# Kernel optimization log

Hardware: AMD Instinct MI355X
Metric: run time of the kernel (lower is better)

## Reference

```python
import jax, jax.numpy as jnp
import numpy as np

B, S, D, H = 4, 2048, 1024, 16
HD = D // H


def setup_inputs() -> dict:
    key = jax.random.key(0)
    ks = jax.random.split(key, 11)
    s = 1.0 / np.sqrt(D)
    inp = {
        "query": jax.random.normal(ks[0], (B, S, D), jnp.float32),
        "key": jax.random.normal(ks[1], (B, S, D), jnp.float32),
        "value": jax.random.normal(ks[2], (B, S, D), jnp.float32),
        "Wq": jax.random.normal(ks[3], (D, D), jnp.float32) * s,
        "bq": jnp.zeros((D,), jnp.float32),
        "Wk": jax.random.normal(ks[4], (D, D), jnp.float32) * s,
        "bk": jnp.zeros((D,), jnp.float32),
        "Wv": jax.random.normal(ks[5], (D, D), jnp.float32) * s,
        "bv": jnp.zeros((D,), jnp.float32),
        "Wo": jax.random.normal(ks[6], (D, D), jnp.float32) * s,
        "bo": jnp.zeros((D,), jnp.float32),
    }
    return inp


def reference(query, key, value, Wq, bq, Wk, bk, Wv, bv, Wo, bo):
    scale = 1.0 / np.sqrt(HD).astype(np.float32)
    # Linear projections (torch Linear: x @ W.T + b), split into heads -> [B,H,S,HD]
    def proj(x, W, b):
        y = x @ W.T + b
        return y.reshape(B, S, H, HD).transpose(0, 2, 1, 3)

    q = proj(query, Wq, bq)
    k = proj(key, Wk, bk)
    v = proj(value, Wv, bv)
    scores = jnp.einsum("bhqd,bhkd->bhqk", q, k) * scale  # [B,H,S,S]
    weights = jax.nn.softmax(scores, axis=-1)
    attn = jnp.einsum("bhqk,bhkd->bhqd", weights, v)
    attn = attn.transpose(0, 2, 1, 3).reshape(B, S, D)
    return attn @ Wo.T + bo
```

## Files before the change

kernel.cpp:

```cpp
#include <hip/hip_runtime.h>
#include <hip/hip_bf16.h>
#include <stdint.h>

#define Bn 4
#define Sn 2048
#define Dn 1024
#define Hn 16
#define HDn 64
#define Mn (Bn * Sn)
#define PS 44

typedef __attribute__((ext_vector_type(8))) __bf16 bf16x8;
typedef __attribute__((ext_vector_type(4))) __bf16 bf16x4;
typedef __attribute__((ext_vector_type(4))) float f32x4;

#if __has_builtin(__builtin_amdgcn_exp2f)
#define EXP2F(x) __builtin_amdgcn_exp2f(x)
#else
#define EXP2F(x) exp2f(x)
#endif

typedef __attribute__((address_space(1))) unsigned int as1_uint;
typedef __attribute__((address_space(3))) unsigned int as3_uint;

__device__ __forceinline__ void gld_lds16(const void* g, void* l) {
  __builtin_amdgcn_global_load_lds((const as1_uint*)g, (as3_uint*)l, 16, 0, 0);
}

struct CvtArgs {
  const float* src[7];
};
__constant__ const size_t kGb[8] = {0,       1048576, 2097152, 3145728,
                                    3276800, 3407872, 3538944, 3670016};

__global__ __launch_bounds__(256) void cvt_all(CvtArgs a, __bf16* __restrict__ dst) {
  size_t i = (size_t)blockIdx.x * 256 + threadIdx.x;
  if (i >= 3670016) return;
  int s = 0;
#pragma unroll
  for (int k = 1; k < 7; k++) s += (i >= kGb[k]) ? 1 : 0;
  const float4* sp = (const float4*)a.src[s] + 2 * (i - kGb[s]);
  float4 x = sp[0], y = sp[1];
  bf16x8 o;
  o[0] = (__bf16)x.x; o[1] = (__bf16)x.y; o[2] = (__bf16)x.z; o[3] = (__bf16)x.w;
  o[4] = (__bf16)y.x; o[5] = (__bf16)y.y; o[6] = (__bf16)y.z; o[7] = (__bf16)y.w;
  *(bf16x8*)(dst + 8 * i) = o;
}

template <int MODE>
__device__ __forceinline__ void gemm128_body(const __bf16* __restrict__ A,
                                             const __bf16* __restrict__ Bw,
                                             const float* __restrict__ bias,
                                             void* __restrict__ Cout, int m0, int n0,
                                             float scale) {
  __shared__ __align__(16) __bf16 lA[128 * 32];
  __shared__ __align__(16) __bf16 lB[128 * 32];
  const int tid = threadIdx.x;
  const int wave = tid >> 6, lane = tid & 63, quad = lane >> 4, l15 = lane & 15;
  const int wm = wave >> 1, wn = wave & 1;
  f32x4 acc[4][4] = {};
  const char* Ab = (const char*)(A + (size_t)m0 * Dn);
  const char* Bb = (const char*)(Bw + (size_t)n0 * Dn);
  char* lAc = (char*)lA;
  char* lBc = (char*)lB;
  const int o0 = tid * 16, o1 = o0 + 4096;
  const int r0 = o0 >> 6, c0 = o0 & 63;
  const int r1 = o1 >> 6, c1 = o1 & 63;

  for (int k0 = 0; k0 < Dn; k0 += 32) {
    __syncthreads();
    gld_lds16(Ab + (size_t)r0 * 2048 + k0 * 2 + c0, lAc + o0);
    gld_lds16(Ab + (size_t)r1 * 2048 + k0 * 2 + c1, lAc + o1);
    gld_lds16(Bb + (size_t)r0 * 2048 + k0 * 2 + c0, lBc + o0);
    gld_lds16(Bb + (size_t)r1 * 2048 + k0 * 2 + c1, lBc + o1);
    __syncthreads();
    bf16x8 af[4], bfv[4];
#pragma unroll
    for (int i = 0; i < 4; i++)
      af[i] = *(const bf16x8*)(lA + (wm * 64 + i * 16 + l15) * 32 + quad * 8);
#pragma unroll
    for (int t = 0; t < 4; t++)
      bfv[t] = *(const bf16x8*)(lB + (wn * 64 + t * 16 + l15) * 32 + quad * 8);
#pragma unroll
    for (int i = 0; i < 4; i++)
#pragma unroll
      for (int t = 0; t < 4; t++)
        acc[i][t] = __builtin_amdgcn_mfma_f32_16x16x32_bf16(af[i], bfv[t], acc[i][t], 0, 0, 0);
  }
#pragma unroll
  for (int i = 0; i < 4; i++) {
    const int rowb = m0 + wm * 64 + i * 16 + quad * 4;
#pragma unroll
    for (int t = 0; t < 4; t++) {
      const int col = n0 + wn * 64 + t * 16 + l15;
      const float bb = bias[col];
      if (MODE == 2) {
        const int b = rowb >> 11, s = rowb & 2047;
        const int h = col >> 6, c = col & 63;
        bf16x4 pk;
#pragma unroll
        for (int r = 0; r < 4; r++) pk[r] = (__bf16)(acc[i][t][r] + bb);
        *(bf16x4*)((__bf16*)Cout + (((size_t)(b * Hn + h) * HDn + c) * Sn + s)) = pk;
      } else {
#pragma unroll
        for (int r = 0; r < 4; r++) {
          float v = (acc[i][t][r] + bb) * scale;
          if (MODE == 1)
            ((float*)Cout)[(size_t)(rowb + r) * Dn + col] = v;
          else
            ((__bf16*)Cout)[(size_t)(rowb + r) * Dn + col] = (__bf16)v;
        }
      }
    }
  }
}

__global__ __launch_bounds__(256, 3) void qkv_gemm(
    const __bf16* __restrict__ X, const __bf16* __restrict__ W,
    const float* __restrict__ bq, const float* __restrict__ bk,
    const float* __restrict__ bv, __bf16* __restrict__ out) {
  const int z = blockIdx.z;
  const int m0 = blockIdx.y * 128, n0 = blockIdx.x * 128;
  if (z == 0) {
    gemm128_body<0>(X, W, bq, out, m0, n0, 0.18033688011112042f);
  } else if (z == 1) {
    gemm128_body<0>(X + (size_t)Mn * Dn, W + (size_t)Dn * Dn, bk,
                    out + (size_t)Mn * Dn, m0, n0, 1.0f);
  } else {
    gemm128_body<2>(X + 2 * (size_t)Mn * Dn, W + 2 * (size_t)Dn * Dn, bv,
                    out + 2 * (size_t)Mn * Dn, m0, n0, 1.0f);
  }
}

__global__ __launch_bounds__(256, 3) void out_gemm(const __bf16* __restrict__ A,
                                                   const __bf16* __restrict__ W,
                                                   const float* __restrict__ bo,
                                                   float* __restrict__ out) {
  gemm128_body<1>(A, W, bo, out, blockIdx.y * 128, blockIdx.x * 128, 1.0f);
}

__global__ __launch_bounds__(256, 2) void flash_attn(const __bf16* __restrict__ Q,
                                                     const __bf16* __restrict__ K,
                                                     const __bf16* __restrict__ Vt,
                                                     __bf16* __restrict__ Aout) {
  __shared__ __align__(16) __bf16 plds[4][64 * PS];
  const int tid = threadIdx.x;
  const int wave = tid >> 6, lane = tid & 63, quad = lane >> 4, l15 = lane & 15;
  const int b = blockIdx.y >> 4, h = blockIdx.y & 15;
  const int q0 = blockIdx.x * 256 + wave * 64;
  const __bf16* Qb = Q + ((size_t)b * Sn) * Dn + h * HDn;
  const __bf16* Kb = K + ((size_t)b * Sn) * Dn + h * HDn;
  const __bf16* Vtb = Vt + (size_t)(b * Hn + h) * HDn * Sn;
  __bf16* myP = &plds[wave][0];

  bf16x8 qf[4][2];
#pragma unroll
  for (int iq = 0; iq < 4; iq++)
#pragma unroll
    for (int s = 0; s < 2; s++)
      qf[iq][s] = *(const bf16x8*)(Qb + (size_t)(q0 + iq * 16 + l15) * Dn + s * 32 + quad * 8);

  f32x4 O[4][4] = {};
  float li[4] = {};

  bf16x8 kf[2][2][2];
  bf16x8 vf[2][4];
#pragma unroll
  for (int tk = 0; tk < 2; tk++)
#pragma unroll
    for (int s = 0; s < 2; s++)
      kf[0][tk][s] = *(const bf16x8*)(Kb + (size_t)(tk * 16 + l15) * Dn + s * 32 + quad * 8);
#pragma unroll
  for (int mc = 0; mc < 4; mc++)
    vf[0][mc] = *(const bf16x8*)(Vtb + (size_t)(mc * 16 + l15) * Sn + quad * 8);

#pragma unroll 2
  for (int kt = 0; kt < Sn / 32; kt++) {
    const int cur = kt & 1, nxt = cur ^ 1;
    f32x4 sa[2][4];
#pragma unroll
    for (int tk = 0; tk < 2; tk++)
#pragma unroll
      for (int iq = 0; iq < 4; iq++) {
        f32x4 z = {0.f, 0.f, 0.f, 0.f};
        z = __builtin_amdgcn_mfma_f32_16x16x32_bf16(kf[cur][tk][0], qf[iq][0], z, 0, 0, 0);
        z = __builtin_amdgcn_mfma_f32_16x16x32_bf16(kf[cur][tk][1], qf[iq][1], z, 0, 0, 0);
        sa[tk][iq] = z;
      }
    if (kt < Sn / 32 - 1) {
      const int key0 = (kt + 1) * 32;
#pragma unroll
      for (int tk = 0; tk < 2; tk++)
#pragma unroll
        for (int s = 0; s < 2; s++)
          kf[nxt][tk][s] =
              *(const bf16x8*)(Kb + (size_t)(key0 + tk * 16 + l15) * Dn + s * 32 + quad * 8);
#pragma unroll
      for (int mc = 0; mc < 4; mc++)
        vf[nxt][mc] = *(const bf16x8*)(Vtb + (size_t)(mc * 16 + l15) * Sn + key0 + quad * 8);
    }
#pragma unroll
    for (int tk = 0; tk < 2; tk++)
#pragma unroll
      for (int iq = 0; iq < 4; iq++) {
        bf16x4 pk;
#pragma unroll
        for (int r = 0; r < 4; r++) {
          float p = EXP2F(sa[tk][iq][r]);
          li[iq] += p;
          pk[r] = (__bf16)p;
        }
        *(bf16x4*)(myP + (iq * 16 + l15) * PS + tk * 16 + quad * 4) = pk;
      }
#pragma unroll
    for (int iq = 0; iq < 4; iq++) {
      bf16x4 plo = *(const bf16x4*)(myP + (iq * 16 + l15) * PS + quad * 8);
      bf16x4 phi = *(const bf16x4*)(myP + (iq * 16 + l15) * PS + quad * 8 + 4);
      bf16x8 pf = __builtin_shufflevector(plo, phi, 0, 1, 2, 3, 4, 5, 6, 7);
#pragma unroll
      for (int mc = 0; mc < 4; mc++)
        O[mc][iq] = __builtin_amdgcn_mfma_f32_16x16x32_bf16(vf[cur][mc], pf, O[mc][iq], 0, 0, 0);
    }
  }
  float inv[4];
#pragma unroll
  for (int iq = 0; iq < 4; iq++) {
    float s = li[iq];
    s += __shfl_xor(s, 16);
    s += __shfl_xor(s, 32);
    inv[iq] = 1.0f / s;
  }
#pragma unroll
  for (int mc = 0; mc < 4; mc++)
#pragma unroll
    for (int iq = 0; iq < 4; iq++) {
      bf16x4 o;
#pragma unroll
      for (int r = 0; r < 4; r++) o[r] = (__bf16)(O[mc][iq][r] * inv[iq]);
      *(bf16x4*)(Aout + ((size_t)b * Sn + q0 + iq * 16 + l15) * Dn + h * HDn + mc * 16 +
                 quad * 4) = o;
    }
}

extern "C" void kernel_launch(void* const* d_in, const int* in_sizes, int n_in,
                              void* d_out, int out_size, void* d_ws, size_t ws_size,
                              hipStream_t stream) {
  const float* bq = (const float*)d_in[4];
  const float* bk = (const float*)d_in[6];
  const float* bv = (const float*)d_in[8];
  const float* bo = (const float*)d_in[10];

  const size_t MD = (size_t)Mn * Dn;
  const size_t DD = (size_t)Dn * Dn;
  __bf16* Xbf  = (__bf16*)d_ws;
  __bf16* Wbf  = Xbf + 3 * MD;
  __bf16* QKV  = Wbf + 4 * DD;
  __bf16* Attn = QKV + 3 * MD;

  CvtArgs ca;
  ca.src[0] = (const float*)d_in[0];
  ca.src[1] = (const float*)d_in[1];
  ca.src[2] = (const float*)d_in[2];
  ca.src[3] = (const float*)d_in[3];
  ca.src[4] = (const float*)d_in[5];
  ca.src[5] = (const float*)d_in[7];
  ca.src[6] = (const float*)d_in[9];
  cvt_all<<<14336, 256, 0, stream>>>(ca, Xbf);

  qkv_gemm<<<dim3(Dn / 128, Mn / 128, 3), 256, 0, stream>>>(Xbf, Wbf, bq, bk, bv, QKV);
  flash_attn<<<dim3(Sn / 256, Bn * Hn), 256, 0, stream>>>(QKV, QKV + MD, QKV + 2 * MD, Attn);
  out_gemm<<<dim3(Dn / 128, Mn / 128), 256, 0, stream>>>(Attn, Wbf + 3 * DD, bo, (float*)d_out);
}
```

Measured before the change: 392.4 us.

## Split attention over key ranges and add a reduction kernel

The flash attention kernel now splits the key range across a grid z dimension when the workspace is large enough. Each split writes unnormalized fp32 partial outputs and row sums, and a new reduce_norm kernel adds them and normalizes to bf16. The V projection is computed as W·X^T, so V^T is stored with a contiguous [H*HD, B*S] layout, and the K/V double-buffer prefetch is simplified. These changes aim to raise parallelism and occupancy in the attention stage. They cost extra fp32 partial traffic, an additional kernel launch, and some reduced latency hiding inside the loop.

```diff
diff --git a/kernel.cpp b/kernel.cpp
--- a/kernel.cpp
+++ b/kernel.cpp
@@ -30,8 +30,8 @@
 struct CvtArgs {
   const float* src[7];
 };
-__constant__ const size_t kGb[8] = {0,       1048576, 2097152, 3145728,
-                                    3276800, 3407872, 3538944, 3670016};
+__constant__ const size_t kGb[8] = {0,      131072,  262144,  393216,
+                                    524288, 1572864, 2621440, 3670016};
 
 __global__ __launch_bounds__(256) void cvt_all(CvtArgs a, __bf16* __restrict__ dst) {
   size_t i = (size_t)blockIdx.x * 256 + threadIdx.x;
@@ -93,15 +93,14 @@
 #pragma unroll
     for (int t = 0; t < 4; t++) {
       const int col = n0 + wn * 64 + t * 16 + l15;
-      const float bb = bias[col];
-      if (MODE == 2) {
-        const int b = rowb >> 11, s = rowb & 2047;
-        const int h = col >> 6, c = col & 63;
-        bf16x4 pk;
-#pragma unroll
-        for (int r = 0; r < 4; r++) pk[r] = (__bf16)(acc[i][t][r] + bb);
-        *(bf16x4*)((__bf16*)Cout + (((size_t)(b * Hn + h) * HDn + c) * Sn + s)) = pk;
+      if (MODE == 3) {
+#pragma unroll
+        for (int r = 0; r < 4; r++) {
+          float v = acc[i][t][r] + bias[rowb + r];
+          ((__bf16*)Cout)[(size_t)(rowb + r) * Mn + col] = (__bf16)v;
+        }
       } else {
+        const float bb = bias[col];
 #pragma unroll
         for (int r = 0; r < 4; r++) {
           float v = (acc[i][t][r] + bb) * scale;
@@ -120,15 +119,15 @@
     const float* __restrict__ bq, const float* __restrict__ bk,
     const float* __restrict__ bv, __bf16* __restrict__ out) {
   const int z = blockIdx.z;
-  const int m0 = blockIdx.y * 128, n0 = blockIdx.x * 128;
+  const size_t MD = (size_t)Mn * Dn, DD = (size_t)Dn * Dn;
   if (z == 0) {
-    gemm128_body<0>(X, W, bq, out, m0, n0, 0.18033688011112042f);
+    gemm128_body<0>(X, W, bq, out, blockIdx.y * 128, blockIdx.x * 128,
+                    0.18033688011112042f);
   } else if (z == 1) {
-    gemm128_body<0>(X + (size_t)Mn * Dn, W + (size_t)Dn * Dn, bk,
-                    out + (size_t)Mn * Dn, m0, n0, 1.0f);
+    gemm128_body<0>(X + MD, W + DD, bk, out + MD, blockIdx.y * 128, blockIdx.x * 128, 1.0f);
   } else {
-    gemm128_body<2>(X + 2 * (size_t)Mn * Dn, W + 2 * (size_t)Dn * Dn, bv,
-                    out + 2 * (size_t)Mn * Dn, m0, n0, 1.0f);
+    gemm128_body<3>(W + 2 * DD, X + 2 * MD, bv, out + 2 * MD, blockIdx.x * 128,
+                    blockIdx.y * 128, 1.0f);
   }
 }
 
@@ -139,18 +138,21 @@
   gemm128_body<1>(A, W, bo, out, blockIdx.y * 128, blockIdx.x * 128, 1.0f);
 }
 
-__global__ __launch_bounds__(256, 2) void flash_attn(const __bf16* __restrict__ Q,
+__global__ __launch_bounds__(256, 3) void flash_attn(const __bf16* __restrict__ Q,
                                                      const __bf16* __restrict__ K,
                                                      const __bf16* __restrict__ Vt,
-                                                     __bf16* __restrict__ Aout) {
+                                                     float* __restrict__ Opart,
+                                                     float* __restrict__ Lpart) {
   __shared__ __align__(16) __bf16 plds[4][64 * PS];
   const int tid = threadIdx.x;
   const int wave = tid >> 6, lane = tid & 63, quad = lane >> 4, l15 = lane & 15;
   const int b = blockIdx.y >> 4, h = blockIdx.y & 15;
   const int q0 = blockIdx.x * 256 + wave * 64;
+  const int split = blockIdx.z, nsp = gridDim.z;
+  const int kspan = Sn / nsp, kbeg = split * kspan;
   const __bf16* Qb = Q + ((size_t)b * Sn) * Dn + h * HDn;
   const __bf16* Kb = K + ((size_t)b * Sn) * Dn + h * HDn;
-  const __bf16* Vtb = Vt + (size_t)(b * Hn + h) * HDn * Sn;
+  const __bf16* Vtb = Vt + (size_t)h * HDn * Mn + b * Sn;
   __bf16* myP = &plds[wave][0];
 
   bf16x8 qf[4][2];
@@ -163,55 +165,50 @@
   f32x4 O[4][4] = {};
   float li[4] = {};
 
-  bf16x8 kf[2][2][2];
-  bf16x8 vf[2][4];
+  bf16x8 kf[2][2];
 #pragma unroll
   for (int tk = 0; tk < 2; tk++)
 #pragma unroll
     for (int s = 0; s < 2; s++)
-      kf[0][tk][s] = *(const bf16x8*)(Kb + (size_t)(tk * 16 + l15) * Dn + s * 32 + quad * 8);
-#pragma unroll
-  for (int mc = 0; mc < 4; mc++)
-    vf[0][mc] = *(const bf16x8*)(Vtb + (size_t)(mc * 16 + l15) * Sn + quad * 8);
-
-#pragma unroll 2
-  for (int kt = 0; kt < Sn / 32; kt++) {
-    const int cur = kt & 1, nxt = cur ^ 1;
-    f32x4 sa[2][4];
-#pragma unroll
-    for (int tk = 0; tk < 2; tk++)
+      kf[tk][s] = *(const bf16x8*)(Kb + (size_t)(kbeg + tk * 16 + l15) * Dn + s * 32 + quad * 8);
+
+  for (int kt = 0; kt < kspan / 32; kt++) {
+    const int key0 = kbeg + kt * 32;
+    bf16x8 vf[4];
+#pragma unroll
+    for (int mc = 0; mc < 4; mc++)
+      vf[mc] = *(const bf16x8*)(Vtb + (size_t)(mc * 16 + l15) * Mn + key0 + quad * 8);
+#pragma unroll
+    for (int tk = 0; tk < 2; tk++) {
+      f32x4 sa[4];
 #pragma unroll
       for (int iq = 0; iq < 4; iq++) {
         f32x4 z = {0.f, 0.f, 0.f, 0.f};
-        z = __builtin_amdgcn_mfma_f32_16x16x32_bf16(kf[cur][tk][0], qf[iq][0], z, 0, 0, 0);
-        z = __builtin_amdgcn_mfma_f32_16x16x32_bf16(kf[cur][tk][1], qf[iq][1], z, 0, 0, 0);
-        sa[tk][iq] = z;
+        z = __builtin_amdgcn_mfma_f32_16x16x32_bf16(kf[tk][0], qf[iq][0], z, 0, 0, 0);
+        z = __builtin_amdgcn_mfma_f32_16x16x32_bf16(kf[tk][1], qf[iq][1], z, 0, 0, 0);
+        sa[iq] = z;
       }
-    if (kt < Sn / 32 - 1) {
-      const int key0 = (kt + 1) * 32;
-#pragma unroll
-      for (int tk = 0; tk < 2; tk++)
-#pragma unroll
-        for (int s = 0; s < 2; s++)
-          kf[nxt][tk][s] =
-              *(const bf16x8*)(Kb + (size_t)(key0 + tk * 16 + l15) * Dn + s * 32 + quad * 8);
-#pragma unroll
-      for (int mc = 0; mc < 4; mc++)
-        vf[nxt][mc] = *(const bf16x8*)(Vtb + (size_t)(mc * 16 + l15) * Sn + key0 + quad * 8);
-    }
-#pragma unroll
-    for (int tk = 0; tk < 2; tk++)
 #pragma unroll
       for (int iq = 0; iq < 4; iq++) {
         bf16x4 pk;
 #pragma unroll
         for (int r = 0; r < 4; r++) {
-          float p = EXP2F(sa[tk][iq][r]);
+          float p = EXP2F(sa[iq][r]);
           li[iq] += p;
           pk[r] = (__bf16)p;
         }
         *(bf16x4*)(myP + (iq * 16 + l15) * PS + tk * 16 + quad * 4) = pk;
       }
+    }
+    if (kt + 1 < kspan / 32) {
+      const int kn = key0 + 32;
+#pragma unroll
+      for (int tk = 0; tk < 2; tk++)
+#pragma unroll
+        for (int s = 0; s < 2; s++)
+          kf[tk][s] =
+              *(const bf16x8*)(Kb + (size_t)(kn + tk * 16 + l15) * Dn + s * 32 + quad * 8);
+    }
 #pragma unroll
     for (int iq = 0; iq < 4; iq++) {
       bf16x4 plo = *(const bf16x4*)(myP + (iq * 16 + l15) * PS + quad * 8);
@@ -219,27 +216,50 @@
       bf16x8 pf = __builtin_shufflevector(plo, phi, 0, 1, 2, 3, 4, 5, 6, 7);
 #pragma unroll
       for (int mc = 0; mc < 4; mc++)
-        O[mc][iq] = __builtin_amdgcn_mfma_f32_16x16x32_bf16(vf[cur][mc], pf, O[mc][iq], 0, 0, 0);
+        O[mc][iq] = __builtin_amdgcn_mfma_f32_16x16x32_bf16(vf[mc], pf, O[mc][iq], 0, 0, 0);
     }
   }
-  float inv[4];
 #pragma unroll
   for (int iq = 0; iq < 4; iq++) {
     float s = li[iq];
     s += __shfl_xor(s, 16);
     s += __shfl_xor(s, 32);
-    inv[iq] = 1.0f / s;
-  }
+    li[iq] = s;
+  }
+  if (quad == 0) {
+#pragma unroll
+    for (int iq = 0; iq < 4; iq++)
+      Lpart[(size_t)split * (Bn * Hn * Sn) + ((size_t)(b * Hn + h)) * Sn + q0 + iq * 16 + l15] =
+          li[iq];
+  }
+  float* Ob = Opart + (size_t)split * Mn * Dn;
 #pragma unroll
   for (int mc = 0; mc < 4; mc++)
 #pragma unroll
-    for (int iq = 0; iq < 4; iq++) {
-      bf16x4 o;
-#pragma unroll
-      for (int r = 0; r < 4; r++) o[r] = (__bf16)(O[mc][iq][r] * inv[iq]);
-      *(bf16x4*)(Aout + ((size_t)b * Sn + q0 + iq * 16 + l15) * Dn + h * HDn + mc * 16 +
-                 quad * 4) = o;
-    }
+    for (int iq = 0; iq < 4; iq++)
+      *(f32x4*)(Ob + ((size_t)b * Sn + q0 + iq * 16 + l15) * Dn + h * HDn + mc * 16 + quad * 4) =
+          O[mc][iq];
+}
+
+__global__ __launch_bounds__(256) void reduce_norm(const float* __restrict__ O,
+                                                   const float* __restrict__ L, int nsplit,
+                                                   __bf16* __restrict__ Attn) {
+  const int m = blockIdx.x, t = threadIdx.x;
+  const int d0 = t * 4, h = d0 >> 6;
+  const int b = m >> 11, q = m & 2047;
+  const size_t lio = ((size_t)(b * Hn + h)) * Sn + q;
+  float l = L[lio];
+  f32x4 o = *(const f32x4*)(O + (size_t)m * Dn + d0);
+  if (nsplit == 2) {
+    l += L[(size_t)Bn * Hn * Sn + lio];
+    f32x4 o2 = *(const f32x4*)(O + (size_t)Mn * Dn + (size_t)m * Dn + d0);
+    o += o2;
+  }
+  const float inv = 1.0f / l;
+  bf16x4 r;
+#pragma unroll
+  for (int k = 0; k < 4; k++) r[k] = (__bf16)(o[k] * inv);
+  *(bf16x4*)(Attn + (size_t)m * Dn + d0) = r;
 }
 
 extern "C" void kernel_launch(void* const* d_in, const int* in_sizes, int n_in,
@@ -252,22 +272,35 @@
 
   const size_t MD = (size_t)Mn * Dn;
   const size_t DD = (size_t)Dn * Dn;
-  __bf16* Xbf  = (__bf16*)d_ws;
-  __bf16* Wbf  = Xbf + 3 * MD;
-  __bf16* QKV  = Wbf + 4 * DD;
-  __bf16* Attn = QKV + 3 * MD;
+  const size_t MB = 1ull << 20;
+  __bf16* Wbf  = (__bf16*)d_ws;
+  __bf16* Xbf  = (__bf16*)((char*)d_ws + 8 * MB);
+  __bf16* QKV  = (__bf16*)((char*)d_ws + 56 * MB);
+  __bf16* Attn = (__bf16*)((char*)d_ws + 104 * MB);
+  const int nsplit = (ws_size >= 186 * MB) ? 2 : 1;
+  float* Lpart;
+  float* Opart;
+  if (nsplit == 2) {
+    Lpart = (float*)((char*)d_ws + 120 * MB);
+    Opart = (float*)((char*)d_ws + 121 * MB);
+  } else {
+    Lpart = (float*)((char*)d_ws + 8 * MB);
+    Opart = (float*)((char*)d_ws + 9 * MB);
+  }
 
   CvtArgs ca;
-  ca.src[0] = (const float*)d_in[0];
-  ca.src[1] = (const float*)d_in[1];
-  ca.src[2] = (const float*)d_in[2];
-  ca.src[3] = (const float*)d_in[3];
-  ca.src[4] = (const float*)d_in[5];
-  ca.src[5] = (const float*)d_in[7];
-  ca.src[6] = (const float*)d_in[9];
-  cvt_all<<<14336, 256, 0, stream>>>(ca, Xbf);
+  ca.src[0] = (const float*)d_in[3];
+  ca.src[1] = (const float*)d_in[5];
+  ca.src[2] = (const float*)d_in[7];
+  ca.src[3] = (const float*)d_in[9];
+  ca.src[4] = (const float*)d_in[0];
+  ca.src[5] = (const float*)d_in[1];
+  ca.src[6] = (const float*)d_in[2];
+  cvt_all<<<14336, 256, 0, stream>>>(ca, Wbf);
 
   qkv_gemm<<<dim3(Dn / 128, Mn / 128, 3), 256, 0, stream>>>(Xbf, Wbf, bq, bk, bv, QKV);
-  flash_attn<<<dim3(Sn / 256, Bn * Hn), 256, 0, stream>>>(QKV, QKV + MD, QKV + 2 * MD, Attn);
+  flash_attn<<<dim3(Sn / 256, Bn * Hn, nsplit), 256, 0, stream>>>(QKV, QKV + MD, QKV + 2 * MD,
+                                                                  Opart, Lpart);
+  reduce_norm<<<Mn, 256, 0, stream>>>(Opart, Lpart, nsplit, Attn);
   out_gemm<<<dim3(Dn / 128, Mn / 128), 256, 0, stream>>>(Attn, Wbf + 3 * DD, bo, (float*)d_out);
 }
```

New measurement: 513.4 us. +30.8%, slower.
